# Kernel tuning notes

Hardware: AMD Instinct MI355X
Metric: run time of the kernel (lower is better)

The kernel has to match this reference:

```python
import jax, jax.numpy as jnp
import numpy as np
from itertools import permutations

NEG = -1e30  # finite 'log-zero' sentinel to keep grads NaN-free
DEN_SCALE = 1.0


def fsm_log_marginal(llh, seqlen, src, dst, pdf, weight, init, final):
    """Log-marginal (total log path weight) of an FSM over a sequence.

    llh: [T, C] frame pdf log-likelihoods; arcs (src,dst,pdf,weight): [A];
    init/final: [N] state log-weights. Forward recursion:
      alpha_{t+1}[j] = logsumexp_{arcs a: dst=j} alpha_t[src_a] + w_a + llh[t, pdf_a]
    Frames t >= seqlen are identity (alpha frozen).
    """
    N = init.shape[0]
    T = llh.shape[0]

    def step(alpha, xs):
        llh_t, t = xs
        score = alpha[src] + weight + llh_t[pdf]  # [A]
        m = jnp.maximum(jax.ops.segment_max(score, dst, num_segments=N), NEG)
        s = jax.ops.segment_sum(jnp.exp(score - m[dst]), dst, num_segments=N)
        new = m + jnp.log(jnp.maximum(s, 1e-30))
        alpha = jnp.where(t < seqlen, new, alpha)
        return alpha, None

    alpha, _ = jax.lax.scan(step, init, (llh, jnp.arange(T)))
    return jax.nn.logsumexp(alpha + final)


# vmap over batch (FSM shared -> None axes) for the denominator
_den_b = jax.vmap(fsm_log_marginal, in_axes=(0, 0, None, None, None, None, None, None))
_den_sb = jax.vmap(_den_b, in_axes=(0, 0, None, None, None, None, None, None))
# vmap over (speaker, batch) with per-(s,b) numerator FSMs
_num_sb = jax.vmap(jax.vmap(fsm_log_marginal))


def reference(est_llhs, seqlengths, den_src, den_dst, den_pdf, den_weight,
              den_init, den_final, num_src, num_dst, num_pdf, num_weight,
              num_init, num_final):
    S = est_llhs.shape[1]
    llhs = jnp.transpose(est_llhs, (1, 0, 2, 3))  # [S, B, T, C]
    seql = seqlengths.T                           # [S, B]

    # denominator: shared graph, summed over speakers -> [B]
    den = _den_sb(llhs, seql, den_src, den_dst, den_pdf, den_weight,
                  den_init, den_final)  # [S, B]
    den_llh = den.sum(axis=0)

    # numerator: evaluate every speaker permutation, take min over perms
    num_per_perm = []
    for p in permutations(range(S)):
        pidx = jnp.array(p)
        nl = _num_sb(llhs[pidx], seql[pidx], num_src, num_dst, num_pdf,
                     num_weight, num_init, num_final)  # [S, B]
        num_per_perm.append(nl.sum(axis=0))
    num_llh = jnp.min(jnp.stack(num_per_perm, axis=1), axis=1)  # [B]

    loss = -(num_llh - DEN_SCALE * den_llh)
    return loss.sum()


def setup_inputs() -> dict:
    key = jax.random.key(0)
    ks = jax.random.split(key, 14)
    B, S, T, C = 8, 2, 512, 2048
    Nd, Ad = 1024, 16384   # denominator graph
    Nn, An = 256, 2048     # numerator graphs (per speaker, per utt)

    est_llhs = jax.nn.log_softmax(
        jax.random.normal(ks[0], (B, S, T, C), jnp.float32), axis=-1)
    seqlengths = jax.random.randint(ks[1], (B, S), T // 2, T + 1, jnp.int32)

    den_src = jax.random.randint(ks[2], (Ad,), 0, Nd, jnp.int32)
    den_dst = jax.random.randint(ks[3], (Ad,), 0, Nd, jnp.int32)
    den_pdf = jax.random.randint(ks[4], (Ad,), 0, C, jnp.int32)
    den_weight = 0.1 * jax.random.normal(ks[5], (Ad,), jnp.float32)
    den_init = jax.nn.log_softmax(jax.random.normal(ks[6], (Nd,), jnp.float32))
    den_final = jax.nn.log_softmax(jax.random.normal(ks[7], (Nd,), jnp.float32))

    num_src = jax.random.randint(ks[8], (S, B, An), 0, Nn, jnp.int32)
    num_dst = jax.random.randint(ks[9], (S, B, An), 0, Nn, jnp.int32)
    num_pdf = jax.random.randint(ks[10], (S, B, An), 0, C, jnp.int32)
    num_weight = 0.1 * jax.random.normal(ks[11], (S, B, An), jnp.float32)
    num_init = jax.nn.log_softmax(
        jax.random.normal(ks[12], (S, B, Nn), jnp.float32), axis=-1)
    num_final = jax.nn.log_softmax(
        jax.random.normal(ks[13], (S, B, Nn), jnp.float32), axis=-1)

    return {
        'est_llhs': est_llhs, 'seqlengths': seqlengths,
        'den_src': den_src, 'den_dst': den_dst, 'den_pdf': den_pdf,
        'den_weight': den_weight, 'den_init': den_init, 'den_final': den_final,
        'num_src': num_src, 'num_dst': num_dst, 'num_pdf': num_pdf,
        'num_weight': num_weight, 'num_init': num_init, 'num_final': num_final,
    }
```

## Files before the change

kernel.cpp:

```cpp
#include <hip/hip_runtime.h>
#include <cstdint>
#include <cstddef>

#define BB 8
#define SS 2
#define TT 512
#define CC 2048
#define ND 1024
#define AD 16384
#define NN 256
#define AN 2048
#define NEGV -1e30f
#define NTH 1024
#define NWG 256

__global__ void prep_kernel(const int* __restrict__ src, const int* __restrict__ dst,
                            const int* __restrict__ pdf, const float* __restrict__ w,
                            unsigned* __restrict__ meta_t, float* __restrict__ w_t,
                            unsigned* __restrict__ pxi,
                            int* __restrict__ pbeg, int* __restrict__ padj,
                            int N, int A, int LC)
{
    __shared__ int cnt[1024];
    __shared__ int pos[1024];
    __shared__ unsigned char gcnt[8192];
    const int g = blockIdx.x;
    src += (size_t)g * A; dst += (size_t)g * A; pdf += (size_t)g * A; w += (size_t)g * A;
    meta_t += (size_t)g * A; w_t += (size_t)g * A; pxi += (size_t)g * A;
    pbeg += (size_t)g * (N + 1); padj += (size_t)g * N;
    const int tid = threadIdx.x;
    cnt[tid] = 0;
    __syncthreads();
    for (int a = tid; a < A; a += blockDim.x) atomicAdd(&cnt[dst[a]], 1);
    __syncthreads();
    const int deg = cnt[tid];
    pos[tid] = deg;
    __syncthreads();
    for (int off = 1; off < blockDim.x; off <<= 1) {
        int add = (tid >= off) ? pos[tid - off] : 0;
        __syncthreads();
        pos[tid] += add;
        __syncthreads();
    }
    const int r0 = pos[tid] - deg;
    const int np = deg ? (((r0 + deg - 1) >> LC) - (r0 >> LC) + 1) : 0;
    __syncthreads();
    pos[tid] = np;
    __syncthreads();
    for (int off = 1; off < blockDim.x; off <<= 1) {
        int add = (tid >= off) ? pos[tid - off] : 0;
        __syncthreads();
        pos[tid] += add;
        __syncthreads();
    }
    const int pexcl = pos[tid] - np;
    pbeg[tid] = pexcl;
    if (tid == blockDim.x - 1) pbeg[N] = pexcl + np;
    padj[tid] = pexcl - (r0 >> LC);
    cnt[tid] = r0;
    __syncthreads();
    for (int a = tid; a < A; a += blockDim.x) {
        const int d2 = dst[a];
        const int p = atomicAdd(&cnt[d2], 1);
        const int l = p >> LC;
        const int i = p & ((1 << LC) - 1);
        meta_t[(size_t)i * NTH + l] = (unsigned)src[a] | ((unsigned)d2 << 16);
        w_t[(size_t)i * NTH + l] = w[a];
        pxi[p] = (unsigned)pdf[a];
    }
    __syncthreads();
    const int CH = 1 << LC;
    const int ngrp = (NTH / 64) * CH;
    if (tid < ngrp) {
        unsigned char* cb = &gcnt[tid * 32];
        for (int b = 0; b < 32; ++b) cb[b] = 0;
        const int i = tid & (CH - 1);
        const int w2 = tid >> LC;
        for (int lane = 0; lane < 64; ++lane) {
            const size_t idx = (size_t)i * NTH + (w2 * 64 + lane);
            const unsigned mt = meta_t[idx];
            const unsigned sv = mt & 0xffffu;
            const unsigned alt = sv ^ ((sv >> 5) & 31u);
            const int b0 = (int)(sv & 31u), b1 = (int)(alt & 31u);
            unsigned gx;
            if (cb[b1] < cb[b0]) { cb[b1]++; gx = (unsigned)N + alt; }
            else                 { cb[b0]++; gx = sv; }
            meta_t[idx] = (mt & 0xffff0000u) | gx;
        }
    }
}

__device__ void wprep_part(int ub, int nb, int t0, int Tt, const float* __restrict__ est,
                           const unsigned* __restrict__ pxi_den,
                           const unsigned* __restrict__ pxi_num,
                           float* __restrict__ Wd, float* __restrict__ Wn,
                           float* row_s)
{
    const int tid = threadIdx.x;
    const int nden = 16 * Tt;
    const int total = nden + 32 * Tt;
    for (int u = ub; u < total; u += nb) {
        __syncthreads();
        const float* row; const unsigned* pxi; float* out; int nar;
        if (u < nden) {
            const int inst = u / Tt, trel = u - inst * Tt;
            const int s = inst >> 3, b = inst & 7;
            row = est + ((size_t)(b * SS + s) * TT + (t0 + trel)) * CC;
            pxi = pxi_den;
            out = Wd + ((size_t)inst * Tt + trel) * AD;
            nar = AD;
        } else {
            const int v = u - nden;
            const int inst = v / Tt, trel = v - inst * Tt;
            const int gg = inst & 15, p = inst >> 4;
            const int s = gg >> 3, b = gg & 7;
            const int sp = p ? (1 - s) : s;
            row = est + ((size_t)(b * SS + sp) * TT + (t0 + trel)) * CC;
            pxi = pxi_num + (size_t)gg * AN;
            out = Wn + ((size_t)inst * Tt + trel) * AN;
            nar = AN;
        }
        row_s[tid] = row[tid]; row_s[tid + 1024] = row[tid + 1024];
        __syncthreads();
        const uint4* p4 = (const uint4*)pxi;
        float4* o4 = (float4*)out;
        const int n4 = nar >> 2;
        for (int k = tid; k < n4; k += 1024) {
            const uint4 pp = p4[k];
            o4[k] = make_float4(row_s[pp.x], row_s[pp.y], row_s[pp.z], row_s[pp.w]);
        }
    }
}

__global__ __launch_bounds__(1024) void wprep0_kernel(
    const float* __restrict__ est,
    const unsigned* __restrict__ pxi_den, const unsigned* __restrict__ pxi_num,
    float* __restrict__ Wd, float* __restrict__ Wn, int t0, int Tt)
{
    __shared__ float row_s[CC];
    wprep_part(blockIdx.x, gridDim.x, t0, Tt, est, pxi_den, pxi_num, Wd, Wn, row_s);
}

template<int CH>
__device__ inline void load_w_row(const float* __restrict__ p, float* dst)
{
    if constexpr (CH == 16) {
        const float4* p4 = (const float4*)p;
        const float4 a = p4[0], b = p4[1], c = p4[2], d = p4[3];
        dst[0]=a.x;  dst[1]=a.y;  dst[2]=a.z;  dst[3]=a.w;
        dst[4]=b.x;  dst[5]=b.y;  dst[6]=b.z;  dst[7]=b.w;
        dst[8]=c.x;  dst[9]=c.y;  dst[10]=c.z; dst[11]=c.w;
        dst[12]=d.x; dst[13]=d.y; dst[14]=d.z; dst[15]=d.w;
    } else {
        const float2 v = *(const float2*)p;
        dst[0] = v.x; dst[1] = v.y;
    }
}

template<int CH>
__device__ void fsm_forward_tile(int N, int L, int t0, int Tt, bool first, bool last,
    const float* __restrict__ Wrow0, int wstride,
    const unsigned* __restrict__ meta_g, const float* __restrict__ w_g,
    const int* __restrict__ pbeg_g, const int* __restrict__ padj_g,
    const float* __restrict__ initv, const float* __restrict__ finalv,
    float* __restrict__ alpha_gl, float* __restrict__ res,
    float* alpha_s, float2* pk)
{
    const int tid = threadIdx.x;
    unsigned meta[CH]; float wreg[CH];
#pragma unroll
    for (int i = 0; i < CH; ++i) {
        meta[i] = meta_g[i * NTH + tid];
        wreg[i] = w_g[i * NTH + tid];
    }
    unsigned segmask = 0;
#pragma unroll
    for (int i = 0; i < CH; ++i) {
        const int di = (int)(meta[i] >> 16);
        const int dn = (i + 1 < CH) ? (int)(meta[i + 1] >> 16) : -1;
        if (di != dn) segmask |= (1u << i);
    }
    const int slot0 = padj_g[meta[0] >> 16] + tid;
    const bool st = tid < N;
    int pb0 = 0, pb1 = 0; float fin = 0.f;
    if (st) {
        const float a0 = first ? initv[tid] : alpha_gl[tid];
        alpha_s[tid] = a0;
        alpha_s[N + (tid ^ ((tid >> 5) & 31))] = a0;
        pb0 = pbeg_g[tid]; pb1 = pbeg_g[tid + 1];
        fin = finalv[tid];
    }
    int tb = L - t0; if (tb > Tt) tb = Tt; if (tb < 0) tb = 0;
    float wc[CH];
    if (tb > 0) load_w_row<CH>(Wrow0 + (size_t)tid * CH, wc);
    __syncthreads();

    for (int trel = 0; trel < tb; ++trel) {
        const bool pre = (trel + 1 < tb);
        float wn[CH];
        if (pre)
            load_w_row<CH>(Wrow0 + (size_t)(trel + 1) * wstride + (size_t)tid * CH, wn);
        float av[CH];
#pragma unroll
        for (int i = 0; i < CH; ++i)
            av[i] = alpha_s[meta[i] & 0xffffu];
        float m = -INFINITY, ss = 0.f;
        int sl = slot0;
#pragma unroll
        for (int i = 0; i < CH; ++i) {
            const float sc = (av[i] + wreg[i]) + wc[i];
            const float d = sc - m;
            const float e = __expf(-fabsf(d));
            if (d > 0.f) { ss = ss * e + 1.f; m = sc; }
            else         { ss += e; }
            if (segmask & (1u << i)) {
                pk[sl] = make_float2(m, ss); ++sl;
                m = -INFINITY; ss = 0.f;
            }
        }
        __syncthreads();
        if (st) {
            float v2;
            const int cnt = pb1 - pb0;
            if (cnt > 0) {
                const float2 P0 = pk[pb0];
                const float2 P1 = pk[cnt > 1 ? pb0 + 1 : pb0];
                const float2 P2 = pk[cnt > 2 ? pb0 + 2 : pb0];
                const float2 P3 = pk[cnt > 3 ? pb0 + 3 : pb0];
                float mm = P0.x, s2 = P0.y;
                if (cnt > 1) {
                    const float d = P1.x - mm; const float e = __expf(-fabsf(d));
                    if (d > 0.f) { s2 = s2 * e + P1.y; mm = P1.x; } else { s2 += P1.y * e; }
                }
                if (cnt > 2) {
                    const float d = P2.x - mm; const float e = __expf(-fabsf(d));
                    if (d > 0.f) { s2 = s2 * e + P2.y; mm = P2.x; } else { s2 += P2.y * e; }
                }
                if (cnt > 3) {
                    const float d = P3.x - mm; const float e = __expf(-fabsf(d));
                    if (d > 0.f) { s2 = s2 * e + P3.y; mm = P3.x; } else { s2 += P3.y * e; }
                }
                for (int q2 = pb0 + 4; q2 < pb1; ++q2) {
                    const float2 Pq = pk[q2];
                    const float d = Pq.x - mm; const float e = __expf(-fabsf(d));
                    if (d > 0.f) { s2 = s2 * e + Pq.y; mm = Pq.x; } else { s2 += Pq.y * e; }
                }
                const float mc  = fmaxf(mm, NEGV);
                const float scs = s2 * __expf(mm - mc);
                v2 = mc + __logf(fmaxf(scs, 1e-30f));
            } else {
                v2 = NEGV + __logf(1e-30f);
            }
            alpha_s[tid] = v2;
            alpha_s[N + (tid ^ ((tid >> 5) & 31))] = v2;
        }
        __syncthreads();
        if (pre) {
#pragma unroll
            for (int i = 0; i < CH; ++i) wc[i] = wn[i];
        }
    }

    if (last) {
        const float v = st ? (alpha_s[tid] + fin) : -INFINITY;
        float* red = (float*)pk;
        red[tid] = v;
        __syncthreads();
        for (int off = 512; off > 0; off >>= 1) {
            if (tid < off) red[tid] = fmaxf(red[tid], red[tid + off]);
            __syncthreads();
        }
        const float M = red[0];
        __syncthreads();
        red[tid] = __expf(v - M);
        __syncthreads();
        for (int off = 512; off > 0; off >>= 1) {
            if (tid < off) red[tid] += red[tid + off];
            __syncthreads();
        }
        if (tid == 0) *res = M + __logf(red[0]);
    } else if (st) {
        alpha_gl[tid] = alpha_s[tid];
    }
}

__global__ __launch_bounds__(1024) void fused_kernel(
    const int* __restrict__ seqlen,
    const float* __restrict__ Wd, const float* __restrict__ Wn,
    const unsigned* __restrict__ den_meta, const float* __restrict__ den_w,
    const int* __restrict__ den_pbeg, const int* __restrict__ den_padj,
    const float* __restrict__ den_init, const float* __restrict__ den_final,
    const unsigned* __restrict__ num_meta, const float* __restrict__ num_w,
    const int* __restrict__ num_pbeg, const int* __restrict__ num_padj,
    const float* __restrict__ num_init, const float* __restrict__ num_final,
    float* __restrict__ alpha_g, float* __restrict__ res,
    int t0, int Tt, int last,
    const float* __restrict__ est,
    const unsigned* __restrict__ pxi_den, const unsigned* __restrict__ pxi_num,
    float* __restrict__ Wd_next, float* __restrict__ Wn_next)
{
    __shared__ float alpha[2048];
    __shared__ float2 pk[2048];
    __shared__ float row_s[CC];
    const int bid = blockIdx.x;
    const bool first = (t0 == 0);
    if (bid >= 48) {
        if (!last)
            wprep_part(bid - 48, NWG - 48, t0 + Tt, Tt, est, pxi_den, pxi_num,
                       Wd_next, Wn_next, row_s);
        return;
    }
    if (bid < 16) {
        const int s = bid >> 3, b = bid & 7;
        const int L = seqlen[b * SS + s];
        fsm_forward_tile<16>(ND, L, t0, Tt, first, last != 0,
                             Wd + (size_t)bid * Tt * AD, AD,
                             den_meta, den_w, den_pbeg, den_padj,
                             den_init, den_final,
                             alpha_g + (size_t)bid * 1024, &res[bid], alpha, pk);
    } else {
        const int q = bid - 16;
        const int p = q >> 4, g = q & 15;
        const int s = g >> 3, b = g & 7;
        const int sp = p ? (1 - s) : s;
        const int L = seqlen[b * SS + sp];
        fsm_forward_tile<2>(NN, L, t0, Tt, first, last != 0,
                            Wn + (size_t)q * Tt * AN, AN,
                            num_meta + (size_t)g * AN, num_w + (size_t)g * AN,
                            num_pbeg + (size_t)g * (NN + 1), num_padj + (size_t)g * NN,
                            num_init + (size_t)g * NN, num_final + (size_t)g * NN,
                            alpha_g + (size_t)bid * 1024, &res[16 + q], alpha, pk);
    }
}

__global__ void finalize_kernel(const float* __restrict__ res, float* __restrict__ out)
{
    if (threadIdx.x == 0 && blockIdx.x == 0) {
        float loss = 0.f;
        for (int b = 0; b < BB; ++b) {
            const float den = res[b] + res[8 + b];
            const float n0  = res[16 + b] + res[16 + 8 + b];
            const float n1  = res[32 + b] + res[32 + 8 + b];
            const float nm  = fminf(n0, n1);
            loss += -(nm - den);
        }
        out[0] = loss;
    }
}

extern "C" void kernel_launch(void* const* d_in, const int* in_sizes, int n_in,
                              void* d_out, int out_size, void* d_ws, size_t ws_size,
                              hipStream_t stream)
{
    const float* est       = (const float*)d_in[0];
    const int*   seqlen    = (const int*)  d_in[1];
    const int*   den_src   = (const int*)  d_in[2];
    const int*   den_dst   = (const int*)  d_in[3];
    const int*   den_pdf   = (const int*)  d_in[4];
    const float* den_w     = (const float*)d_in[5];
    const float* den_init  = (const float*)d_in[6];
    const float* den_final = (const float*)d_in[7];
    const int*   num_src   = (const int*)  d_in[8];
    const int*   num_dst   = (const int*)  d_in[9];
    const int*   num_pdf   = (const int*)  d_in[10];
    const float* num_w     = (const float*)d_in[11];
    const float* num_init  = (const float*)d_in[12];
    const float* num_final = (const float*)d_in[13];

    char* ws = (char*)d_ws;
    unsigned* den_meta = (unsigned*)(ws + 0);
    float*    den_wt   = (float*)   (ws + 65536);
    unsigned* num_meta = (unsigned*)(ws + 131072);
    float*    num_wt   = (float*)   (ws + 262144);
    unsigned* den_pxi  = (unsigned*)(ws + 393216);
    unsigned* num_pxi  = (unsigned*)(ws + 458752);
    int*      den_pbeg = (int*)     (ws + 589824);
    int*      num_pbeg = (int*)     (ws + 594176);
    int*      den_padj = (int*)     (ws + 610816);
    int*      num_padj = (int*)     (ws + 614912);
    float*    alpha_g  = (float*)   (ws + 631296);
    float*    res      = (float*)   (ws + 827904);
    const size_t fixed = 828416;

    int Tt = 64;
    while (Tt > 4 && fixed + 2ull * (size_t)Tt * 1310720ull > ws_size) Tt >>= 1;
    const size_t wbuf_f = (size_t)Tt * (16 * AD + 32 * AN);
    float* Wd0 = (float*)(ws + fixed);
    float* Wn0 = Wd0 + (size_t)16 * Tt * AD;
    float* Wd1 = Wd0 + wbuf_f;
    float* Wn1 = Wd1 + (size_t)16 * Tt * AD;

    prep_kernel<<<1, 1024, 0, stream>>>(den_src, den_dst, den_pdf, den_w,
                                        den_meta, den_wt, den_pxi,
                                        den_pbeg, den_padj, ND, AD, 4);
    prep_kernel<<<16, 256, 0, stream>>>(num_src, num_dst, num_pdf, num_w,
                                        num_meta, num_wt, num_pxi,
                                        num_pbeg, num_padj, NN, AN, 1);

    wprep0_kernel<<<256, 1024, 0, stream>>>(est, den_pxi, num_pxi, Wd0, Wn0, 0, Tt);

    const int nt = TT / Tt;
    for (int k = 0; k < nt; ++k) {
        float* WdC = (k & 1) ? Wd1 : Wd0;
        float* WnC = (k & 1) ? Wn1 : Wn0;
        float* WdN = (k & 1) ? Wd0 : Wd1;
        float* WnN = (k & 1) ? Wn0 : Wn1;
        fused_kernel<<<NWG, 1024, 0, stream>>>(seqlen, WdC, WnC,
                                               den_meta, den_wt, den_pbeg, den_padj,
                                               den_init, den_final,
                                               num_meta, num_wt, num_pbeg, num_padj,
                                               num_init, num_final,
                                               alpha_g, res, k * Tt, Tt,
                                               (k == nt - 1) ? 1 : 0,
                                               est, den_pxi, num_pxi, WdN, WnN);
    }

    finalize_kernel<<<1, 64, 0, stream>>>(res, (float*)d_out);
}
```

Measured before the change: 1.351 ms.

## Restructure denominator FSM forward with dst-sorted balanced arc blocks and in-register segment reduction

The denominator graph is now laid out by a new prep kernel that sorts arcs by destination and splits them into per-wave balanced chunks of 20 arcs per thread, with padding. Each thread finishes its segments directly and writes alpha into a double-buffered shared array. Segments that cross thread boundaries are merged through wavefront shuffles, which drops the shared packed-partials pass and one barrier per frame. The cost is a larger padded weight buffer (20K vs 16K entries per frame), more registers per thread, and a more intricate prep step that assumes each segment spans at most three neighbouring threads.

```diff
diff --git a/kernel.cpp b/kernel.cpp
--- a/kernel.cpp
+++ b/kernel.cpp
@@ -13,6 +13,12 @@
 #define NEGV -1e30f
 #define NTH 1024
 #define NWG 256
+#define BP 20
+#define ADP (BP * 1024)
+
+#define LSE_MERGE(mm, s2, m2, sp) do { \
+    const float _d = (m2) - (mm); const float _e = __expf(-fabsf(_d)); \
+    if (_d > 0.f) { s2 = s2 * _e + (sp); mm = (m2); } else { s2 += (sp) * _e; } } while (0)
 
 __global__ void prep_kernel(const int* __restrict__ src, const int* __restrict__ dst,
                             const int* __restrict__ pdf, const float* __restrict__ w,
@@ -90,6 +96,124 @@
     }
 }
 
+__global__ __launch_bounds__(1024) void prep_den_kernel(
+    const int* __restrict__ src, const int* __restrict__ dst,
+    const int* __restrict__ pdf, const float* __restrict__ w,
+    unsigned* __restrict__ meta_t, float* __restrict__ w_t,
+    unsigned* __restrict__ pxi, unsigned* __restrict__ flg,
+    unsigned* __restrict__ tst, unsigned* __restrict__ deg0m)
+{
+    __shared__ int cnt[1024];
+    __shared__ int pos[1024];
+    __shared__ int rp[1025];
+    __shared__ int wb[17];
+    __shared__ unsigned char gcnt[16 * BP * 32];
+    const int tid = threadIdx.x;
+    cnt[tid] = 0;
+    __syncthreads();
+    for (int a = tid; a < AD; a += 1024) atomicAdd(&cnt[dst[a]], 1);
+    __syncthreads();
+    const int deg = cnt[tid];
+    pos[tid] = deg;
+    __syncthreads();
+    for (int off = 1; off < 1024; off <<= 1) {
+        int add = (tid >= off) ? pos[tid - off] : 0;
+        __syncthreads();
+        pos[tid] += add;
+        __syncthreads();
+    }
+    rp[tid + 1] = pos[tid];
+    if (tid == 0) rp[0] = 0;
+    __syncthreads();
+    if (tid < 32) {
+        unsigned mw = 0;
+        for (int b = 0; b < 32; ++b)
+            if (rp[tid * 32 + b + 1] == rp[tid * 32 + b]) mw |= (1u << b);
+        deg0m[tid] = mw;
+    }
+    if (tid == 0) {
+        int j = 0;
+        wb[0] = 0;
+        for (int wv = 0; wv < 16; ++wv) {
+            if (wv == 15) { j = 1024; }
+            else {
+                const int rem = AD - rp[j];
+                const int target = (rem + (15 - wv)) / (16 - wv);
+                int acc = 0;
+                while (j < 1024 && acc < target) { acc += rp[j + 1] - rp[j]; ++j; }
+            }
+            wb[wv + 1] = rp[j];
+        }
+    }
+    __syncthreads();
+    for (int p = tid; p < ADP; p += 1024) {
+        meta_t[p] = 0xFFFFFFFFu;
+        w_t[p] = -1e38f;
+        pxi[p] = 0u;
+    }
+    cnt[tid] = rp[tid];
+    __syncthreads();
+    for (int a = tid; a < AD; a += 1024) {
+        const int d2 = dst[a];
+        const int p = atomicAdd(&cnt[d2], 1);
+        int wv = 0;
+        while (p >= wb[wv + 1]) ++wv;
+        const int rel = p - wb[wv];
+        const int l = (wv << 6) + rel / BP;
+        const int i = rel % BP;
+        meta_t[i * NTH + l] = (unsigned)src[a] | ((unsigned)d2 << 16);
+        w_t[i * NTH + l] = w[a];
+        pxi[l * BP + i] = (unsigned)pdf[a];
+    }
+    __syncthreads();
+    {
+        const int wv = tid >> 6;
+        const int base = wb[wv], end = wb[wv + 1];
+        int o0 = base + BP * (tid & 63); if (o0 > end) o0 = end;
+        int o1 = base + BP * ((tid & 63) + 1); if (o1 > end) o1 = end;
+        const int cl = o1 - o0;
+        unsigned segm = 0;
+        int prevd = -1, lastd = 0;
+        for (int i = 0; i < cl; ++i) {
+            const int d2 = (int)((meta_t[i * NTH + tid] >> 16) & 0x3FFu);
+            if (i > 0 && d2 != prevd) segm |= (1u << (i - 1));
+            prevd = d2; lastd = d2;
+        }
+        unsigned fic = 0;
+        if (cl > 0 && o0 > base) {
+            const int dprev = (int)((meta_t[(BP - 1) * NTH + (tid - 1)] >> 16) & 0x3FFu);
+            const int d0x   = (int)((meta_t[0 * NTH + tid] >> 16) & 0x3FFu);
+            if (dprev == d0x) fic = 1;
+        }
+        unsigned pcv = 0;
+        if (cl > 0) {
+            const int rend = rp[lastd + 1];
+            if (rend > o1) { pcv = (unsigned)((rend - o1 + BP - 1) / BP); if (pcv > 3u) pcv = 3u; }
+        }
+        flg[tid] = segm | (fic << 19) | (pcv << 21) | ((unsigned)cl << 23);
+        tst[tid] = (unsigned)lastd;
+    }
+    __syncthreads();
+    if (tid < 16 * BP) {
+        unsigned char* cb = &gcnt[tid * 32];
+        for (int b = 0; b < 32; ++b) cb[b] = 0;
+        const int i = tid % BP;
+        const int wv = tid / BP;
+        for (int lane = 0; lane < 64; ++lane) {
+            const int idx = i * NTH + ((wv << 6) + lane);
+            const unsigned mt = meta_t[idx];
+            if (mt == 0xFFFFFFFFu) { meta_t[idx] = 0u; continue; }
+            const unsigned sv = mt & 0xFFFFu;
+            const unsigned alt = sv ^ ((sv >> 5) & 31u);
+            const int b0 = (int)(sv & 31u), b1 = (int)(alt & 31u);
+            unsigned gx;
+            if (cb[b1] < cb[b0]) { cb[b1]++; gx = 1024u + alt; }
+            else                 { cb[b0]++; gx = sv; }
+            meta_t[idx] = (mt & 0xFFFF0000u) | gx;
+        }
+    }
+}
+
 __device__ void wprep_part(int ub, int nb, int t0, int Tt, const float* __restrict__ est,
                            const unsigned* __restrict__ pxi_den,
                            const unsigned* __restrict__ pxi_num,
@@ -107,8 +231,8 @@
             const int s = inst >> 3, b = inst & 7;
             row = est + ((size_t)(b * SS + s) * TT + (t0 + trel)) * CC;
             pxi = pxi_den;
-            out = Wd + ((size_t)inst * Tt + trel) * AD;
-            nar = AD;
+            out = Wd + ((size_t)inst * Tt + trel) * ADP;
+            nar = ADP;
         } else {
             const int v = u - nden;
             const int inst = v / Tt, trel = v - inst * Tt;
@@ -141,19 +265,132 @@
     wprep_part(blockIdx.x, gridDim.x, t0, Tt, est, pxi_den, pxi_num, Wd, Wn, row_s);
 }
 
-template<int CH>
-__device__ inline void load_w_row(const float* __restrict__ p, float* dst)
-{
-    if constexpr (CH == 16) {
-        const float4* p4 = (const float4*)p;
-        const float4 a = p4[0], b = p4[1], c = p4[2], d = p4[3];
-        dst[0]=a.x;  dst[1]=a.y;  dst[2]=a.z;  dst[3]=a.w;
-        dst[4]=b.x;  dst[5]=b.y;  dst[6]=b.z;  dst[7]=b.w;
-        dst[8]=c.x;  dst[9]=c.y;  dst[10]=c.z; dst[11]=c.w;
-        dst[12]=d.x; dst[13]=d.y; dst[14]=d.z; dst[15]=d.w;
+__device__ void fsm_forward_den(int L, int t0, int Tt, bool first, bool last,
+    const float* __restrict__ Wrow0,
+    const unsigned* __restrict__ meta_g, const float* __restrict__ w_g,
+    const unsigned* __restrict__ flg_g, const unsigned* __restrict__ tst_g,
+    const unsigned* __restrict__ deg0m,
+    const float* __restrict__ initv, const float* __restrict__ finalv,
+    float* __restrict__ alpha_gl, float* __restrict__ res,
+    float* bufA, float* bufB, float* red)
+{
+    const int tid = threadIdx.x;
+    unsigned meta[BP]; float wreg[BP];
+#pragma unroll
+    for (int i = 0; i < BP; ++i) {
+        meta[i] = meta_g[i * NTH + tid];
+        wreg[i] = w_g[i * NTH + tid];
+    }
+    const unsigned fl = flg_g[tid];
+    const unsigned segm = fl & 0x7FFFFu;
+    const unsigned fic  = (fl >> 19) & 1u;
+    const unsigned pc   = (fl >> 21) & 3u;
+    const int      cl   = (int)(fl >> 23);
+    const bool     own  = (cl > 0) && !(fic && segm == 0u);
+    const unsigned wmask = fic ? (segm & (segm - 1u)) : segm;
+    const int tstate = (int)tst_g[tid];
+    const int tdual  = 1024 + (tstate ^ ((tstate >> 5) & 31));
+    const int sdual  = 1024 + (tid ^ ((tid >> 5) & 31));
+    const unsigned d0 = (deg0m[tid >> 5] >> (tid & 31)) & 1u;
+    const float c0 = NEGV + __logf(1e-30f);
+    const float fin = finalv[tid];
+
+    const float a0 = first ? initv[tid] : alpha_gl[tid];
+    bufA[tid] = a0;
+    bufA[sdual] = a0;
+    int tb = L - t0; if (tb > Tt) tb = Tt; if (tb < 0) tb = 0;
+    float wc[BP];
+    if (tb > 0) {
+        const float* p = Wrow0 + (size_t)tid * BP;
+#pragma unroll
+        for (int q = 0; q < BP / 4; ++q) {
+            const float4 v = ((const float4*)p)[q];
+            wc[4*q] = v.x; wc[4*q+1] = v.y; wc[4*q+2] = v.z; wc[4*q+3] = v.w;
+        }
+    }
+    __syncthreads();
+
+    float* cur = bufA; float* nxt = bufB;
+    for (int trel = 0; trel < tb; ++trel) {
+        const bool pre = (trel + 1 < tb);
+        float wn[BP];
+        if (pre) {
+            const float* p = Wrow0 + (size_t)(trel + 1) * ADP + (size_t)tid * BP;
+#pragma unroll
+            for (int q = 0; q < BP / 4; ++q) {
+                const float4 v = ((const float4*)p)[q];
+                wn[4*q] = v.x; wn[4*q+1] = v.y; wn[4*q+2] = v.z; wn[4*q+3] = v.w;
+            }
+        }
+        float av[BP];
+#pragma unroll
+        for (int i = 0; i < BP; ++i) av[i] = cur[meta[i] & 0xFFFFu];
+        float m = -INFINITY, ss = 0.f;
+        float hm = 0.f, hs = 0.f;
+        bool hcap = false;
+#pragma unroll
+        for (int i = 0; i < BP; ++i) {
+            const float sc = (av[i] + wreg[i]) + wc[i];
+            const float d = sc - m;
+            const float e = __expf(-fabsf(d));
+            if (d > 0.f) { ss = ss * e + 1.f; m = sc; }
+            else         { ss += e; }
+            if (segm & (1u << i)) {
+                if (!hcap) { hm = m; hs = ss; hcap = true; }
+                if (wmask & (1u << i)) {
+                    const float mc  = fmaxf(m, NEGV);
+                    const float scs = ss * __expf(m - mc);
+                    const float v2  = mc + __logf(fmaxf(scs, 1e-30f));
+                    const int dj = (int)((meta[i] >> 16) & 0x3FFu);
+                    nxt[dj] = v2;
+                    nxt[1024 + (dj ^ ((dj >> 5) & 31))] = v2;
+                }
+                m = -INFINITY; ss = 0.f;
+            }
+        }
+        if (!hcap) { hm = m; hs = ss; }
+        const float h1m = __shfl_down(hm, 1), h1s = __shfl_down(hs, 1);
+        const float h2m = __shfl_down(hm, 2), h2s = __shfl_down(hs, 2);
+        const float h3m = __shfl_down(hm, 3), h3s = __shfl_down(hs, 3);
+        float tm = m, ts = ss;
+        if (pc >= 1u) LSE_MERGE(tm, ts, h1m, h1s);
+        if (pc >= 2u) LSE_MERGE(tm, ts, h2m, h2s);
+        if (pc >= 3u) LSE_MERGE(tm, ts, h3m, h3s);
+        if (own) {
+            const float mc  = fmaxf(tm, NEGV);
+            const float scs = ts * __expf(tm - mc);
+            const float v2  = mc + __logf(fmaxf(scs, 1e-30f));
+            nxt[tstate] = v2;
+            nxt[tdual]  = v2;
+        }
+        if (d0) { nxt[tid] = c0; nxt[sdual] = c0; }
+        __syncthreads();
+        float* t2 = cur; cur = nxt; nxt = t2;
+        if (pre) {
+#pragma unroll
+            for (int i = 0; i < BP; ++i) wc[i] = wn[i];
+        }
+    }
+
+    if (last) {
+        const float v = cur[tid] + fin;
+        red[tid] = v;
+        __syncthreads();
+        for (int off = 512; off > 0; off >>= 1) {
+            if (tid < off) red[tid] = fmaxf(red[tid], red[tid + off]);
+            __syncthreads();
+        }
+        const float M = red[0];
+        __syncthreads();
+        red[tid] = __expf(v - M);
+        __syncthreads();
+        for (int off = 512; off > 0; off >>= 1) {
+            if (tid < off) red[tid] += red[tid + off];
+            __syncthreads();
+        }
+        if (tid == 0) *res = M + __logf(red[0]);
     } else {
-        const float2 v = *(const float2*)p;
-        dst[0] = v.x; dst[1] = v.y;
+        alpha_gl[tid] = cur[tid];
     }
 }
 
@@ -192,18 +429,22 @@
     }
     int tb = L - t0; if (tb > Tt) tb = Tt; if (tb < 0) tb = 0;
     float wc[CH];
-    if (tb > 0) load_w_row<CH>(Wrow0 + (size_t)tid * CH, wc);
+    if (tb > 0) {
+        const float2 v = *(const float2*)(Wrow0 + (size_t)tid * CH);
+        wc[0] = v.x; wc[1] = v.y;
+    }
     __syncthreads();
 
     for (int trel = 0; trel < tb; ++trel) {
         const bool pre = (trel + 1 < tb);
         float wn[CH];
-        if (pre)
-            load_w_row<CH>(Wrow0 + (size_t)(trel + 1) * wstride + (size_t)tid * CH, wn);
+        if (pre) {
+            const float2 v = *(const float2*)(Wrow0 + (size_t)(trel + 1) * wstride + (size_t)tid * CH);
+            wn[0] = v.x; wn[1] = v.y;
+        }
         float av[CH];
 #pragma unroll
-        for (int i = 0; i < CH; ++i)
-            av[i] = alpha_s[meta[i] & 0xffffu];
+        for (int i = 0; i < CH; ++i) av[i] = alpha_s[meta[i] & 0xffffu];
         float m = -INFINITY, ss = 0.f;
         int sl = slot0;
 #pragma unroll
@@ -221,29 +462,13 @@
         __syncthreads();
         if (st) {
             float v2;
-            const int cnt = pb1 - pb0;
-            if (cnt > 0) {
+            const int cnt2 = pb1 - pb0;
+            if (cnt2 > 0) {
                 const float2 P0 = pk[pb0];
-                const float2 P1 = pk[cnt > 1 ? pb0 + 1 : pb0];
-                const float2 P2 = pk[cnt > 2 ? pb0 + 2 : pb0];
-                const float2 P3 = pk[cnt > 3 ? pb0 + 3 : pb0];
                 float mm = P0.x, s2 = P0.y;
-                if (cnt > 1) {
-                    const float d = P1.x - mm; const float e = __expf(-fabsf(d));
-                    if (d > 0.f) { s2 = s2 * e + P1.y; mm = P1.x; } else { s2 += P1.y * e; }
-                }
-                if (cnt > 2) {
-                    const float d = P2.x - mm; const float e = __expf(-fabsf(d));
-                    if (d > 0.f) { s2 = s2 * e + P2.y; mm = P2.x; } else { s2 += P2.y * e; }
-                }
-                if (cnt > 3) {
-                    const float d = P3.x - mm; const float e = __expf(-fabsf(d));
-                    if (d > 0.f) { s2 = s2 * e + P3.y; mm = P3.x; } else { s2 += P3.y * e; }
-                }
-                for (int q2 = pb0 + 4; q2 < pb1; ++q2) {
+                for (int q2 = pb0 + 1; q2 < pb1; ++q2) {
                     const float2 Pq = pk[q2];
-                    const float d = Pq.x - mm; const float e = __expf(-fabsf(d));
-                    if (d > 0.f) { s2 = s2 * e + Pq.y; mm = Pq.x; } else { s2 += Pq.y * e; }
+                    LSE_MERGE(mm, s2, Pq.x, Pq.y);
                 }
                 const float mc  = fmaxf(mm, NEGV);
                 const float scs = s2 * __expf(mm - mc);
@@ -255,10 +480,7 @@
             alpha_s[N + (tid ^ ((tid >> 5) & 31))] = v2;
         }
         __syncthreads();
-        if (pre) {
-#pragma unroll
-            for (int i = 0; i < CH; ++i) wc[i] = wn[i];
-        }
+        if (pre) { wc[0] = wn[0]; wc[1] = wn[1]; }
     }
 
     if (last) {
@@ -288,7 +510,8 @@
     const int* __restrict__ seqlen,
     const float* __restrict__ Wd, const float* __restrict__ Wn,
     const unsigned* __restrict__ den_meta, const float* __restrict__ den_w,
-    const int* __restrict__ den_pbeg, const int* __restrict__ den_padj,
+    const unsigned* __restrict__ den_flg, const unsigned* __restrict__ den_tst,
+    const unsigned* __restrict__ den_deg0,
     const float* __restrict__ den_init, const float* __restrict__ den_final,
     const unsigned* __restrict__ num_meta, const float* __restrict__ num_w,
     const int* __restrict__ num_pbeg, const int* __restrict__ num_padj,
@@ -299,7 +522,8 @@
     const unsigned* __restrict__ pxi_den, const unsigned* __restrict__ pxi_num,
     float* __restrict__ Wd_next, float* __restrict__ Wn_next)
 {
-    __shared__ float alpha[2048];
+    __shared__ float bufA[2048];
+    __shared__ float bufB[2048];
     __shared__ float2 pk[2048];
     __shared__ float row_s[CC];
     const int bid = blockIdx.x;
@@ -313,11 +537,12 @@
     if (bid < 16) {
         const int s = bid >> 3, b = bid & 7;
         const int L = seqlen[b * SS + s];
-        fsm_forward_tile<16>(ND, L, t0, Tt, first, last != 0,
-                             Wd + (size_t)bid * Tt * AD, AD,
-                             den_meta, den_w, den_pbeg, den_padj,
-                             den_init, den_final,
-                             alpha_g + (size_t)bid * 1024, &res[bid], alpha, pk);
+        fsm_forward_den(L, t0, Tt, first, last != 0,
+                        Wd + (size_t)bid * Tt * ADP,
+                        den_meta, den_w, den_flg, den_tst, den_deg0,
+                        den_init, den_final,
+                        alpha_g + (size_t)bid * 1024, &res[bid],
+                        bufA, bufB, (float*)pk);
     } else {
         const int q = bid - 16;
         const int p = q >> 4, g = q & 15;
@@ -329,7 +554,7 @@
                             num_meta + (size_t)g * AN, num_w + (size_t)g * AN,
                             num_pbeg + (size_t)g * (NN + 1), num_padj + (size_t)g * NN,
                             num_init + (size_t)g * NN, num_final + (size_t)g * NN,
-                            alpha_g + (size_t)bid * 1024, &res[16 + q], alpha, pk);
+                            alpha_g + (size_t)bid * 1024, &res[16 + q], bufA, pk);
     }
 }
 
@@ -369,30 +594,31 @@
 
     char* ws = (char*)d_ws;
     unsigned* den_meta = (unsigned*)(ws + 0);
-    float*    den_wt   = (float*)   (ws + 65536);
-    unsigned* num_meta = (unsigned*)(ws + 131072);
-    float*    num_wt   = (float*)   (ws + 262144);
-    unsigned* den_pxi  = (unsigned*)(ws + 393216);
-    unsigned* num_pxi  = (unsigned*)(ws + 458752);
-    int*      den_pbeg = (int*)     (ws + 589824);
-    int*      num_pbeg = (int*)     (ws + 594176);
-    int*      den_padj = (int*)     (ws + 610816);
-    int*      num_padj = (int*)     (ws + 614912);
-    float*    alpha_g  = (float*)   (ws + 631296);
-    float*    res      = (float*)   (ws + 827904);
-    const size_t fixed = 828416;
+    float*    den_wt   = (float*)   (ws + 81920);
+    unsigned* num_meta = (unsigned*)(ws + 163840);
+    float*    num_wt   = (float*)   (ws + 294912);
+    unsigned* den_pxi  = (unsigned*)(ws + 425984);
+    unsigned* num_pxi  = (unsigned*)(ws + 507904);
+    int*      num_pbeg = (int*)     (ws + 638976);
+    int*      num_padj = (int*)     (ws + 655424);
+    unsigned* den_flg  = (unsigned*)(ws + 671808);
+    unsigned* den_tst  = (unsigned*)(ws + 675904);
+    unsigned* den_deg0 = (unsigned*)(ws + 680000);
+    float*    alpha_g  = (float*)   (ws + 680128);
+    float*    res      = (float*)   (ws + 876736);
+    const size_t fixed = 877056;
 
     int Tt = 64;
-    while (Tt > 4 && fixed + 2ull * (size_t)Tt * 1310720ull > ws_size) Tt >>= 1;
-    const size_t wbuf_f = (size_t)Tt * (16 * AD + 32 * AN);
+    while (Tt > 4 && fixed + 2ull * (size_t)Tt * 1572864ull > ws_size) Tt >>= 1;
+    const size_t wbuf_f = (size_t)Tt * (16 * ADP + 32 * AN);
     float* Wd0 = (float*)(ws + fixed);
-    float* Wn0 = Wd0 + (size_t)16 * Tt * AD;
+    float* Wn0 = Wd0 + (size_t)16 * Tt * ADP;
     float* Wd1 = Wd0 + wbuf_f;
-    float* Wn1 = Wd1 + (size_t)16 * Tt * AD;
-
-    prep_kernel<<<1, 1024, 0, stream>>>(den_src, den_dst, den_pdf, den_w,
-                                        den_meta, den_wt, den_pxi,
-                                        den_pbeg, den_padj, ND, AD, 4);
+    float* Wn1 = Wd1 + (size_t)16 * Tt * ADP;
+
+    prep_den_kernel<<<1, 1024, 0, stream>>>(den_src, den_dst, den_pdf, den_w,
+                                            den_meta, den_wt, den_pxi,
+                                            den_flg, den_tst, den_deg0);
     prep_kernel<<<16, 256, 0, stream>>>(num_src, num_dst, num_pdf, num_w,
                                         num_meta, num_wt, num_pxi,
                                         num_pbeg, num_padj, NN, AN, 1);
@@ -406,7 +632,7 @@
         float* WdN = (k & 1) ? Wd0 : Wd1;
         float* WnN = (k & 1) ? Wn0 : Wn1;
         fused_kernel<<<NWG, 1024, 0, stream>>>(seqlen, WdC, WnC,
-                                               den_meta, den_wt, den_pbeg, den_padj,
+                                               den_meta, den_wt, den_flg, den_tst, den_deg0,
                                                den_init, den_final,
                                                num_meta, num_wt, num_pbeg, num_padj,
                                                num_init, num_final,
```

Result: slower. 2.622 ms (+94.2%).
